# Performance work log

Measured on AMD Instinct MI355X. Metric: run time of the kernel, lower is better.

The kernel has to match this reference:

```python
import jax, jax.numpy as jnp
import numpy as np
import math

DIM = 1024
K = 3
NUM_LAYERS = 1
RES_SCALE = 1.0 / math.sqrt(NUM_LAYERS)


def rmsnorm(x, gamma):
    # F.normalize(x, dim=-1) * sqrt(dim) * (gamma + 1)
    n = jnp.sqrt(jnp.sum(x * x, axis=-1, keepdims=True))
    return x / jnp.maximum(n, 1e-12) * (x.shape[-1] ** 0.5) * (gamma + 1.0)


def causal_dwconv(x, w_dw, b_dw, w_pw, b_pw):
    # x: [B, L, D]; w_dw: [D, 1, K]; w_pw: [D, D]
    xt = jnp.transpose(x, (0, 2, 1))                     # [B, D, L]
    xt = jnp.pad(xt, ((0, 0), (0, 0), (K - 1, 0)))       # causal left pad
    y = jax.lax.conv_general_dilated(
        xt, w_dw, window_strides=(1,), padding='VALID',
        feature_group_count=xt.shape[1],
        dimension_numbers=('NCH', 'OIH', 'NCH'))          # [B, D, L]
    y = y + b_dw[None, :, None]
    y = jnp.transpose(y, (0, 2, 1))                       # [B, L, D]
    return jnp.einsum('bld,ed->ble', y, w_pw) + b_pw      # 1x1 conv


def log_g(x):
    return jnp.where(x >= 0, jnp.log(jax.nn.relu(x) + 0.5), -jax.nn.softplus(-x))


def heinsen_scan_log(log_coeffs, log_values):
    # h_t = exp(a*_t + logcumsumexp(log_values - a*))
    a_star = jnp.cumsum(log_coeffs, axis=1)
    log_h = a_star + jax.lax.cumlogsumexp(log_values - a_star, axis=1)
    return jnp.exp(log_h)


def min_gru(x, w_hg):
    # x: [B, L, D]; w_hg: [2D, D] (no bias, expansion_factor=1 -> to_out is identity)
    hg = jnp.einsum('bld,ed->ble', x, w_hg)
    hidden, gate = jnp.split(hg, 2, axis=-1)
    log_coeffs = -jax.nn.softplus(gate)        # log(1 - z)
    log_values = -jax.nn.softplus(-gate) + log_g(hidden)  # log z + log g(h~)
    out = heinsen_scan_log(log_coeffs, log_values)         # [B, L, D]
    next_hidden = out[:, -1:]
    return out, next_hidden


def setup_inputs() -> dict:
    key = jax.random.key(0)
    ks = jax.random.split(key, 12)
    D = DIM
    s = 0.02
    return {
        'x': jax.random.normal(ks[0], (4, 4096, D), jnp.float32),
        'conv_dw_w': jax.random.normal(ks[1], (D, 1, K), jnp.float32) * s,
        'conv_dw_b': jax.random.normal(ks[2], (D,), jnp.float32) * s,
        'conv_pw_w': jax.random.normal(ks[3], (D, D), jnp.float32) * s,
        'conv_pw_b': jax.random.normal(ks[4], (D,), jnp.float32) * s,
        'conv_norm_g': jax.random.normal(ks[5], (D,), jnp.float32) * s,
        'gru_norm_g': jax.random.normal(ks[6], (D,), jnp.float32) * s,
        'gru_w': jax.random.normal(ks[7], (2 * D, D), jnp.float32) * s,
        'ff_norm_g': jax.random.normal(ks[8], (D,), jnp.float32) * s,
        'ff_w1': jax.random.normal(ks[9], (4 * D, D), jnp.float32) * s,
        'ff_b1': jax.random.normal(ks[10], (4 * D,), jnp.float32) * s,
        'ff_w2': jax.random.normal(ks[11], (D, 4 * D), jnp.float32) * s,
        'ff_b2': jnp.zeros((D,), jnp.float32),
    }


def reference(x, conv_dw_w, conv_dw_b, conv_pw_w, conv_pw_b, conv_norm_g,
              gru_norm_g, gru_w, ff_norm_g, ff_w1, ff_b1, ff_w2, ff_b2):
    # Conv branch (residual)
    x = causal_dwconv(rmsnorm(x, conv_norm_g), conv_dw_w, conv_dw_b,
                      conv_pw_w, conv_pw_b) * RES_SCALE + x
    # MinGRU branch (residual); dropout is identity at inference
    gru_out, next_hidden = min_gru(rmsnorm(x, gru_norm_g), gru_w)
    x = gru_out * RES_SCALE + x
    # FeedForward branch (residual), exact GELU
    h = rmsnorm(x, ff_norm_g)
    h = jax.nn.gelu(jnp.einsum('bld,ed->ble', h, ff_w1) + ff_b1, approximate=False)
    h = jnp.einsum('ble,de->bld', h, ff_w2) + ff_b2
    x = h * RES_SCALE + x
    return x, next_hidden
```

## Files before the change

kernel.cpp:

```cpp
#include <hip/hip_runtime.h>

typedef __attribute__((ext_vector_type(8))) short short8;
typedef __attribute__((ext_vector_type(4))) float floatx4;

#define D_   1024
#define L_   4096
#define B_   4
#define T_   16384
#define NCH  32
#define CHL  128

__device__ __forceinline__ ushort f2bf(float f) {
  unsigned u = __float_as_uint(f);
  u += 0x7fffu + ((u >> 16) & 1u);
  return (ushort)(u >> 16);
}
__device__ __forceinline__ float bf2f(ushort u) {
  return __uint_as_float(((unsigned)u) << 16);
}

__device__ __forceinline__ void gl2lds(const ushort* g, ushort* l) {
  __builtin_amdgcn_global_load_lds(
      (const __attribute__((address_space(1))) unsigned int*)g,
      (__attribute__((address_space(3))) unsigned int*)l, 16, 0, 0);
}

__global__ __launch_bounds__(256) void cvt_bf(const float* __restrict__ s,
                                              ushort* __restrict__ d, int n4) {
  int i = blockIdx.x * 256 + threadIdx.x;
  if (i >= n4) return;
  float4 v = ((const float4*)s)[i];
  ushort4 o;
  o.x = f2bf(v.x); o.y = f2bf(v.y); o.z = f2bf(v.z); o.w = f2bf(v.w);
  ((ushort4*)d)[i] = o;
}

__global__ __launch_bounds__(256) void rms_scale(const float* __restrict__ x,
                                                 const float* __restrict__ g,
                                                 ushort* __restrict__ z) {
  int t = blockIdx.x;
  float4 v = ((const float4*)(x + (size_t)t * D_))[threadIdx.x];
  float s = v.x * v.x + v.y * v.y + v.z * v.z + v.w * v.w;
#pragma unroll
  for (int off = 32; off > 0; off >>= 1) s += __shfl_xor(s, off, 64);
  __shared__ float red[4];
  if ((threadIdx.x & 63) == 0) red[threadIdx.x >> 6] = s;
  __syncthreads();
  float iv = 32.0f / fmaxf(sqrtf(red[0] + red[1] + red[2] + red[3]), 1e-12f);
  float4 gg = ((const float4*)g)[threadIdx.x];
  ushort4 o;
  o.x = f2bf(v.x * iv * (gg.x + 1.f));
  o.y = f2bf(v.y * iv * (gg.y + 1.f));
  o.z = f2bf(v.z * iv * (gg.z + 1.f));
  o.w = f2bf(v.w * iv * (gg.w + 1.f));
  ((ushort4*)(z + (size_t)t * D_))[threadIdx.x] = o;
}

__global__ __launch_bounds__(256) void dwconv_k(const float* __restrict__ x,
                                                const float* __restrict__ wdw,
                                                const float* __restrict__ bdw,
                                                const float* __restrict__ gm,
                                                ushort* __restrict__ y) {
  int t = blockIdx.x;
  int c4 = threadIdx.x << 2;
  int l = t & (L_ - 1);
  const float* p0 = x + (size_t)t * D_ + c4;
  float4 v0 = *(const float4*)p0;
  float4 v1 = {0.f, 0.f, 0.f, 0.f}, v2 = {0.f, 0.f, 0.f, 0.f};
  if (l >= 1) v1 = *(const float4*)(p0 - D_);
  if (l >= 2) v2 = *(const float4*)(p0 - 2 * D_);
  float s0 = v0.x * v0.x + v0.y * v0.y + v0.z * v0.z + v0.w * v0.w;
  float s1 = v1.x * v1.x + v1.y * v1.y + v1.z * v1.z + v1.w * v1.w;
  float s2 = v2.x * v2.x + v2.y * v2.y + v2.z * v2.z + v2.w * v2.w;
#pragma unroll
  for (int off = 32; off > 0; off >>= 1) {
    s0 += __shfl_xor(s0, off, 64);
    s1 += __shfl_xor(s1, off, 64);
    s2 += __shfl_xor(s2, off, 64);
  }
  __shared__ float r0[4], r1[4], r2[4];
  if ((threadIdx.x & 63) == 0) {
    int w = threadIdx.x >> 6;
    r0[w] = s0; r1[w] = s1; r2[w] = s2;
  }
  __syncthreads();
  float i0 = 32.0f / fmaxf(sqrtf(r0[0] + r0[1] + r0[2] + r0[3]), 1e-12f);
  float i1 = 32.0f / fmaxf(sqrtf(r1[0] + r1[1] + r1[2] + r1[3]), 1e-12f);
  float i2 = 32.0f / fmaxf(sqrtf(r2[0] + r2[1] + r2[2] + r2[3]), 1e-12f);
  float a0[4] = {v0.x, v0.y, v0.z, v0.w};
  float a1[4] = {v1.x, v1.y, v1.z, v1.w};
  float a2[4] = {v2.x, v2.y, v2.z, v2.w};
  ushort r[4];
#pragma unroll
  for (int j = 0; j < 4; ++j) {
    int d = c4 + j;
    float w0 = wdw[d * 3 + 0], w1 = wdw[d * 3 + 1], w2 = wdw[d * 3 + 2];
    float s = w2 * a0[j] * i0 + w1 * a1[j] * i1 + w0 * a2[j] * i2;
    s = s * (gm[d] + 1.0f) + bdw[d];
    r[j] = f2bf(s);
  }
  ushort4 o; o.x = r[0]; o.y = r[1]; o.z = r[2]; o.w = r[3];
  *(ushort4*)(y + (size_t)t * D_ + c4) = o;
}

template <int MODE>
__global__ __launch_bounds__(256, 2) void gemm_k(
    const ushort* __restrict__ A, const ushort* __restrict__ W,
    const float* __restrict__ bias, const float* __restrict__ resid,
    float* __restrict__ outF, ushort* __restrict__ outB, int M, int N, int K) {
  __shared__ ushort lA[128 * 32];
  __shared__ ushort lB[128 * 32];
  int tid = threadIdx.x;

  int nx = gridDim.x;
  int lxs = 31 - __clz(nx);
  int lin = blockIdx.x + blockIdx.y * nx;
  int c = lin & 7, q = lin >> 3;
  int by = (c * (gridDim.y >> 3)) + (q >> lxs);
  int bx = q & (nx - 1);
  int bm = by * 128;
  int bn = bx * 128;

  int wave = tid >> 6, lane = tid & 63;
  int wm = (wave & 1) << 6, wn = (wave >> 1) << 6;
  int row = tid >> 2, kc = (tid & 3) << 3;
  const ushort* pa0 = A + (size_t)(bm + row) * K + kc;
  const ushort* pa1 = pa0 + (size_t)64 * K;
  const ushort* pb0 = W + (size_t)(bn + row) * K + kc;
  const ushort* pb1 = pb0 + (size_t)64 * K;
  ushort* dA0 = lA + tid * 8;
  ushort* dA1 = dA0 + 64 * 32;
  ushort* dB0 = lB + tid * 8;
  ushort* dB1 = dB0 + 64 * 32;
  int fr = lane & 15, fq = lane >> 4;

  floatx4 acc[4][4];
#pragma unroll
  for (int i = 0; i < 4; ++i)
#pragma unroll
    for (int j = 0; j < 4; ++j) acc[i][j] = {0.f, 0.f, 0.f, 0.f};

  for (int k0 = 0; k0 < K; k0 += 32) {
    __syncthreads();
    gl2lds(pa0 + k0, dA0);
    gl2lds(pa1 + k0, dA1);
    gl2lds(pb0 + k0, dB0);
    gl2lds(pb1 + k0, dB1);
    __syncthreads();
    short8 af[4], bfr[4];
#pragma unroll
    for (int i = 0; i < 4; ++i)
      af[i] = *(const short8*)(lA + (wm + i * 16 + fr) * 32 + fq * 8);
#pragma unroll
    for (int j = 0; j < 4; ++j)
      bfr[j] = *(const short8*)(lB + (wn + j * 16 + fr) * 32 + fq * 8);
#pragma unroll
    for (int i = 0; i < 4; ++i)
#pragma unroll
      for (int j = 0; j < 4; ++j)
        acc[i][j] = __builtin_amdgcn_mfma_f32_16x16x32_bf16(af[i], bfr[j], acc[i][j], 0, 0, 0);
  }

#pragma unroll
  for (int i = 0; i < 4; ++i) {
#pragma unroll
    for (int j = 0; j < 4; ++j) {
      int colg = bn + wn + j * 16 + fr;
      float bv = (MODE == 4) ? 0.f : bias[colg];
#pragma unroll
      for (int r = 0; r < 4; ++r) {
        int rowg = bm + wm + i * 16 + fq * 4 + r;
        size_t idx = (size_t)rowg * N + colg;
        float v = acc[i][j][r];
        if (MODE == 0) {
          outF[idx] = v + bv + resid[idx];
        } else if (MODE == 2) {
          v += bv;
          float u = 1.5957691216f * (v + 0.044715f * v * v * v);
          v = v / (1.f + __expf(-u));
          outB[idx] = f2bf(v);
        } else {
          float o;
          if (colg < 1024)
            o = (v >= 0.f) ? (v + 0.5f) : (1.f / (1.f + __expf(-v)));
          else
            o = 1.f / (1.f + __expf(v));
          outB[idx] = f2bf(o);
        }
      }
    }
  }
}

__global__ __launch_bounds__(256) void scan_p1(const ushort* __restrict__ hg,
                                               float* __restrict__ Ag,
                                               float* __restrict__ Bg) {
  int blk = blockIdx.x;
  int dt = blk & 3, ch = (blk >> 2) & 31, b = blk >> 7;
  int d = (dt << 8) + threadIdx.x;
  const ushort* p = hg + (size_t)(b * L_ + ch * CHL) * 2048 + d;
  float A = 1.f, Bv = 0.f;
  for (int s = 0; s < CHL; ++s) {
    float g = bf2f(p[0]), a = bf2f(p[1024]);
    p += 2048;
    A *= a;
    Bv = fmaf(a, Bv, (1.f - a) * g);
  }
  size_t o = (size_t)((b * NCH + ch) * D_) + d;
  Ag[o] = A; Bg[o] = Bv;
}

__global__ __launch_bounds__(256) void scan_p2(const float* __restrict__ Ag,
                                               const float* __restrict__ Bg,
                                               float* __restrict__ Pre) {
  int dt = blockIdx.x & 3, b = blockIdx.x >> 2;
  int d = (dt << 8) + threadIdx.x;
  float h = 0.f;
  for (int c = 0; c < NCH; ++c) {
    size_t i = (size_t)((b * NCH + c) * D_) + d;
    Pre[i] = h;
    h = fmaf(Ag[i], h, Bg[i]);
  }
}

__global__ __launch_bounds__(256) void scan_p3(const ushort* __restrict__ hg,
                                               const float* __restrict__ Pre,
                                               float* __restrict__ xio,
                                               float* __restrict__ nh) {
  int blk = blockIdx.x;
  int dt = blk & 3, ch = (blk >> 2) & 31, b = blk >> 7;
  int d = (dt << 8) + threadIdx.x;
  const ushort* p = hg + (size_t)(b * L_ + ch * CHL) * 2048 + d;
  float* q = xio + (size_t)(b * L_ + ch * CHL) * D_ + d;
  float h = Pre[(size_t)((b * NCH + ch) * D_) + d];
  for (int s = 0; s < CHL; ++s) {
    float g = bf2f(p[0]), a = bf2f(p[1024]);
    p += 2048;
    h = fmaf(a, h, (1.f - a) * g);
    *q = h + *q;
    q += D_;
  }
  if (ch == NCH - 1) nh[(b << 10) + d] = h;
}

extern "C" void kernel_launch(void* const* d_in, const int* in_sizes, int n_in,
                              void* d_out, int out_size, void* d_ws, size_t ws_size,
                              hipStream_t stream) {
  const float* x   = (const float*)d_in[0];
  const float* cdw = (const float*)d_in[1];
  const float* cdb = (const float*)d_in[2];
  const float* cpw = (const float*)d_in[3];
  const float* cpb = (const float*)d_in[4];
  const float* cng = (const float*)d_in[5];
  const float* gng = (const float*)d_in[6];
  const float* gw  = (const float*)d_in[7];
  const float* fng = (const float*)d_in[8];
  const float* fw1 = (const float*)d_in[9];
  const float* fb1 = (const float*)d_in[10];
  const float* fw2 = (const float*)d_in[11];
  const float* fb2 = (const float*)d_in[12];
  float* out = (float*)d_out;
  char* ws = (char*)d_ws;

  ushort* wpw_b = (ushort*)(ws + 0);
  ushort* wgr_b = (ushort*)(ws + 2097152);
  ushort* wf1_b = (ushort*)(ws + 6291456);
  ushort* wf2_b = (ushort*)(ws + 14680064);
  float*  Ag    = (float*) (ws + 23134208);
  float*  Bg    = (float*) (ws + 23658496);
  float*  Pre   = (float*) (ws + 24182784);
  ushort* zbuf  = (ushort*)(ws + 24707072);
  ushort* hg    = (ushort*)(ws + 58261504);
  ushort* h1    = (ushort*)(ws + 58261504);
  float*  nh    = out + (size_t)T_ * D_;

  cvt_bf<<<dim3(1024), 256, 0, stream>>>(cpw, wpw_b, 262144);
  cvt_bf<<<dim3(2048), 256, 0, stream>>>(gw,  wgr_b, 524288);
  cvt_bf<<<dim3(4096), 256, 0, stream>>>(fw1, wf1_b, 1048576);
  cvt_bf<<<dim3(4096), 256, 0, stream>>>(fw2, wf2_b, 1048576);

  dwconv_k<<<dim3(T_), 256, 0, stream>>>(x, cdw, cdb, cng, zbuf);
  gemm_k<0><<<dim3(8, 128), 256, 0, stream>>>(zbuf, wpw_b, cpb, x, out, nullptr, T_, 1024, 1024);

  rms_scale<<<dim3(T_), 256, 0, stream>>>(out, gng, zbuf);
  gemm_k<4><<<dim3(16, 128), 256, 0, stream>>>(zbuf, wgr_b, nullptr, nullptr, nullptr, hg, T_, 2048, 1024);
  scan_p1<<<dim3(512), 256, 0, stream>>>(hg, Ag, Bg);
  scan_p2<<<dim3(16), 256, 0, stream>>>(Ag, Bg, Pre);
  scan_p3<<<dim3(512), 256, 0, stream>>>(hg, Pre, out, nh);

  rms_scale<<<dim3(T_), 256, 0, stream>>>(out, fng, zbuf);
  gemm_k<2><<<dim3(32, 128), 256, 0, stream>>>(zbuf, wf1_b, fb1, nullptr, nullptr, h1, T_, 4096, 1024);
  gemm_k<0><<<dim3(8, 128), 256, 0, stream>>>(h1, wf2_b, fb2, out, out, nullptr, T_, 1024, 4096);
}
```

Measured before the change: 741.2 us.

## Replace 128x128 GEMM with 256x256 double-buffered swizzled MFMA pipeline

Replaces the simple 128x128, BK=32 GEMM (synchronous load then compute) with a 256x256 tile, BK=64 kernel using 512 threads. It double-buffers LDS with staged global_load_lds, uses XOR-swizzled LDS layouts to avoid bank conflicts, and interleaves partial loads with MFMA quarters under explicit barriers and setprio. The goal is to hide memory latency and raise data reuse per tile. In exchange it uses 128KB of LDS and more accumulator registers, which may limit occupancy, and it yields fewer blocks per GEMM.

```diff
diff --git a/kernel.cpp b/kernel.cpp
--- a/kernel.cpp
+++ b/kernel.cpp
@@ -103,79 +103,185 @@
   *(ushort4*)(y + (size_t)t * D_ + c4) = o;
 }
 
+
+#define READ_A(BUFO, MQ)                                                      \
+  _Pragma("unroll") for (int mf_ = 0; mf_ < 4; ++mf_) {                       \
+    av[2 * mf_]     = *(const short8*)(pA + (BUFO) + (MQ) + mf_ * 1024 + o0); \
+    av[2 * mf_ + 1] = *(const short8*)(pA + (BUFO) + (MQ) + mf_ * 1024 + o1); \
+  }
+
+#define READ_B(BUFO, NH)                                                      \
+  _Pragma("unroll") for (int nf_ = 0; nf_ < 2; ++nf_) {                       \
+    bv[(NH) * 4 + 2 * nf_] =                                                  \
+        *(const short8*)(pB + (BUFO) + (NH) * 2048 + nf_ * 1024 + o0);        \
+    bv[(NH) * 4 + 2 * nf_ + 1] =                                              \
+        *(const short8*)(pB + (BUFO) + (NH) * 2048 + nf_ * 1024 + o1);        \
+  }
+
+#define MFMA_Q(MB, NB)                                                        \
+  __builtin_amdgcn_s_setprio(1);                                              \
+  _Pragma("unroll") for (int mf_ = 0; mf_ < 4; ++mf_) {                       \
+    _Pragma("unroll") for (int nf_ = 0; nf_ < 2; ++nf_) {                     \
+      floatx4 c_ = acc[(MB) + mf_][(NB) + nf_];                               \
+      c_ = __builtin_amdgcn_mfma_f32_16x16x32_bf16(                           \
+          av[2 * mf_], bv[((NB) + nf_) * 2], c_, 0, 0, 0);                    \
+      c_ = __builtin_amdgcn_mfma_f32_16x16x32_bf16(                           \
+          av[2 * mf_ + 1], bv[((NB) + nf_) * 2 + 1], c_, 0, 0, 0);            \
+      acc[(MB) + mf_][(NB) + nf_] = c_;                                       \
+    }                                                                         \
+  }                                                                           \
+  __builtin_amdgcn_s_setprio(0)
+
+#define BAR_LGKM()                                    \
+  __builtin_amdgcn_s_barrier();                       \
+  asm volatile("s_waitcnt lgkmcnt(0)" ::: "memory");  \
+  __builtin_amdgcn_sched_barrier(0)
+
+#define BAR_END()               \
+  __builtin_amdgcn_s_barrier(); \
+  __builtin_amdgcn_sched_barrier(0)
+
 template <int MODE>
-__global__ __launch_bounds__(256, 2) void gemm_k(
+__global__ __launch_bounds__(512, 2) void gemm256(
     const ushort* __restrict__ A, const ushort* __restrict__ W,
     const float* __restrict__ bias, const float* __restrict__ resid,
     float* __restrict__ outF, ushort* __restrict__ outB, int M, int N, int K) {
-  __shared__ ushort lA[128 * 32];
-  __shared__ ushort lB[128 * 32];
-  int tid = threadIdx.x;
-
-  int nx = gridDim.x;
-  int lxs = 31 - __clz(nx);
-  int lin = blockIdx.x + blockIdx.y * nx;
-  int c = lin & 7, q = lin >> 3;
-  int by = (c * (gridDim.y >> 3)) + (q >> lxs);
-  int bx = q & (nx - 1);
-  int bm = by * 128;
-  int bn = bx * 128;
-
-  int wave = tid >> 6, lane = tid & 63;
-  int wm = (wave & 1) << 6, wn = (wave >> 1) << 6;
-  int row = tid >> 2, kc = (tid & 3) << 3;
-  const ushort* pa0 = A + (size_t)(bm + row) * K + kc;
-  const ushort* pa1 = pa0 + (size_t)64 * K;
-  const ushort* pb0 = W + (size_t)(bn + row) * K + kc;
-  const ushort* pb1 = pb0 + (size_t)64 * K;
-  ushort* dA0 = lA + tid * 8;
-  ushort* dA1 = dA0 + 64 * 32;
-  ushort* dB0 = lB + tid * 8;
-  ushort* dB1 = dB0 + 64 * 32;
-  int fr = lane & 15, fq = lane >> 4;
-
-  floatx4 acc[4][4];
-#pragma unroll
-  for (int i = 0; i < 4; ++i)
+  __shared__ ushort lds[65536];
+  const int tid = threadIdx.x;
+
+  const int nx = gridDim.x;
+  const int lxs = 31 - __clz(nx);
+  const int lin = blockIdx.x + blockIdx.y * nx;
+  const int cpx = nx << 3;
+  const int wg = (lin & 7) * cpx + (lin >> 3);
+  const int bm = (wg >> lxs) << 8;
+  const int bn = (wg & (nx - 1)) << 8;
+
+  const int lane = tid & 63, wave = tid >> 6;
+  const int wm = (wave >> 2) & 1;
+  const int wn = wave & 3;
+  const int fr = lane & 15, fq = lane >> 4;
+
+  const int srow = tid >> 3;
+  const int kcs = (tid & 7) ^ (srow & 7);
+  const ushort* gA = A + (size_t)(bm + srow) * K + kcs * 8;
+  const ushort* gB = W + (size_t)(bn + srow) * K + kcs * 8;
+  ushort* ldst = lds + tid * 8;
+
+  const ushort* pA = lds + (size_t)(wm * 128 + fr) * 64;
+  const ushort* pB = lds + 16384 + (size_t)(wn * 64 + fr) * 64;
+  const int o0 = (fq ^ (fr & 7)) * 8;
+  const int o1 = o0 ^ 32;
+
+  floatx4 acc[8][4];
+#pragma unroll
+  for (int i = 0; i < 8; ++i)
 #pragma unroll
     for (int j = 0; j < 4; ++j) acc[i][j] = {0.f, 0.f, 0.f, 0.f};
-
-  for (int k0 = 0; k0 < K; k0 += 32) {
-    __syncthreads();
-    gl2lds(pa0 + k0, dA0);
-    gl2lds(pa1 + k0, dA1);
-    gl2lds(pb0 + k0, dB0);
-    gl2lds(pb1 + k0, dB1);
-    __syncthreads();
-    short8 af[4], bfr[4];
-#pragma unroll
-    for (int i = 0; i < 4; ++i)
-      af[i] = *(const short8*)(lA + (wm + i * 16 + fr) * 32 + fq * 8);
-#pragma unroll
-    for (int j = 0; j < 4; ++j)
-      bfr[j] = *(const short8*)(lB + (wn + j * 16 + fr) * 32 + fq * 8);
-#pragma unroll
-    for (int i = 0; i < 4; ++i)
-#pragma unroll
-      for (int j = 0; j < 4; ++j)
-        acc[i][j] = __builtin_amdgcn_mfma_f32_16x16x32_bf16(af[i], bfr[j], acc[i][j], 0, 0, 0);
-  }
-
-#pragma unroll
-  for (int i = 0; i < 4; ++i) {
-#pragma unroll
-    for (int j = 0; j < 4; ++j) {
-      int colg = bn + wn + j * 16 + fr;
-      float bv = (MODE == 4) ? 0.f : bias[colg];
+  short8 av[8], bv[8];
+
+  auto stageA = [&](int buf, int half, int kt) {
+    const ushort* s = gA + (size_t)(half * 128) * K + kt * 64;
+    ushort* d = ldst + buf * 32768 + half * 8192;
+    gl2lds(s, d);
+    gl2lds(s + (size_t)64 * K, d + 4096);
+  };
+  auto stageB = [&](int buf, int half, int kt) {
+    const ushort* s = gB + (size_t)(half * 128) * K + kt * 64;
+    ushort* d = ldst + buf * 32768 + 16384 + half * 8192;
+    gl2lds(s, d);
+    gl2lds(s + (size_t)64 * K, d + 4096);
+  };
+
+  const int nt = K >> 6;
+
+  stageA(0, 0, 0); stageA(0, 1, 0);
+  stageB(0, 0, 0); stageB(0, 1, 0);
+  stageB(1, 0, 1); stageB(1, 1, 1);
+  asm volatile("s_waitcnt vmcnt(4)" ::: "memory");
+  __builtin_amdgcn_s_barrier();
+  __builtin_amdgcn_sched_barrier(0);
+
+  for (int m = 0; m < nt; m += 2) {
+    const bool more = (m + 2 < nt);
+    READ_A(0, 0);
+    READ_B(0, 0);
+    stageA(1, 0, m + 1);
+    BAR_LGKM();
+    MFMA_Q(0, 0);
+    BAR_END();
+
+    READ_B(0, 1);
+    stageA(1, 1, m + 1);
+    BAR_LGKM();
+    MFMA_Q(0, 2);
+    BAR_END();
+
+    READ_A(0, 4096);
+    if (more) stageB(0, 0, m + 2);
+    BAR_LGKM();
+    MFMA_Q(4, 2);
+    BAR_END();
+
+    if (more) {
+      stageB(0, 1, m + 2);
+      asm volatile("s_waitcnt vmcnt(4)" ::: "memory");
+    } else {
+      asm volatile("s_waitcnt vmcnt(0)" ::: "memory");
+    }
+    __builtin_amdgcn_s_barrier();
+    __builtin_amdgcn_sched_barrier(0);
+    MFMA_Q(4, 0);
+    BAR_END();
+
+    READ_A(32768, 0);
+    READ_B(32768, 0);
+    if (more) stageA(0, 0, m + 2);
+    BAR_LGKM();
+    MFMA_Q(0, 0);
+    BAR_END();
+
+    READ_B(32768, 1);
+    if (more) stageA(0, 1, m + 2);
+    BAR_LGKM();
+    MFMA_Q(0, 2);
+    BAR_END();
+
+    READ_A(32768, 4096);
+    if (more) stageB(1, 0, m + 3);
+    BAR_LGKM();
+    MFMA_Q(4, 2);
+    BAR_END();
+
+    if (more) {
+      stageB(1, 1, m + 3);
+      asm volatile("s_waitcnt vmcnt(4)" ::: "memory");
+    } else {
+      asm volatile("s_waitcnt vmcnt(0)" ::: "memory");
+    }
+    __builtin_amdgcn_s_barrier();
+    __builtin_amdgcn_sched_barrier(0);
+    MFMA_Q(4, 0);
+    BAR_END();
+  }
+
+  const int rowb = bm + wm * 128 + fq * 4;
+  const int colb = bn + wn * 64 + fr;
+#pragma unroll
+  for (int nf = 0; nf < 4; ++nf) {
+    const int colg = colb + nf * 16;
+    const float bvs = (MODE == 4) ? 0.f : bias[colg];
+#pragma unroll
+    for (int mf = 0; mf < 8; ++mf) {
 #pragma unroll
       for (int r = 0; r < 4; ++r) {
-        int rowg = bm + wm + i * 16 + fq * 4 + r;
-        size_t idx = (size_t)rowg * N + colg;
-        float v = acc[i][j][r];
+        const int rowg = rowb + mf * 16 + r;
+        const size_t idx = (size_t)rowg * N + colg;
+        float v = acc[mf][nf][r];
         if (MODE == 0) {
-          outF[idx] = v + bv + resid[idx];
+          outF[idx] = v + bvs + resid[idx];
         } else if (MODE == 2) {
-          v += bv;
+          v += bvs;
           float u = 1.5957691216f * (v + 0.044715f * v * v * v);
           v = v / (1.f + __expf(-u));
           outB[idx] = f2bf(v);
@@ -280,15 +386,15 @@
   cvt_bf<<<dim3(4096), 256, 0, stream>>>(fw2, wf2_b, 1048576);
 
   dwconv_k<<<dim3(T_), 256, 0, stream>>>(x, cdw, cdb, cng, zbuf);
-  gemm_k<0><<<dim3(8, 128), 256, 0, stream>>>(zbuf, wpw_b, cpb, x, out, nullptr, T_, 1024, 1024);
+  gemm256<0><<<dim3(4, 64), 512, 0, stream>>>(zbuf, wpw_b, cpb, x, out, nullptr, T_, 1024, 1024);
 
   rms_scale<<<dim3(T_), 256, 0, stream>>>(out, gng, zbuf);
-  gemm_k<4><<<dim3(16, 128), 256, 0, stream>>>(zbuf, wgr_b, nullptr, nullptr, nullptr, hg, T_, 2048, 1024);
+  gemm256<4><<<dim3(8, 64), 512, 0, stream>>>(zbuf, wgr_b, nullptr, nullptr, nullptr, hg, T_, 2048, 1024);
   scan_p1<<<dim3(512), 256, 0, stream>>>(hg, Ag, Bg);
   scan_p2<<<dim3(16), 256, 0, stream>>>(Ag, Bg, Pre);
   scan_p3<<<dim3(512), 256, 0, stream>>>(hg, Pre, out, nh);
 
   rms_scale<<<dim3(T_), 256, 0, stream>>>(out, fng, zbuf);
-  gemm_k<2><<<dim3(32, 128), 256, 0, stream>>>(zbuf, wf1_b, fb1, nullptr, nullptr, h1, T_, 4096, 1024);
-  gemm_k<0><<<dim3(8, 128), 256, 0, stream>>>(h1, wf2_b, fb2, out, out, nullptr, T_, 1024, 4096);
-}
+  gemm256<2><<<dim3(16, 64), 512, 0, stream>>>(zbuf, wf1_b, fb1, nullptr, nullptr, h1, T_, 4096, 1024);
+  gemm256<0><<<dim3(4, 64), 512, 0, stream>>>(h1, wf2_b, fb2, out, out, nullptr, T_, 1024, 4096);
+}
```

Measured after the change: 715.3 us. -3.5%, faster.
